# Kernel tuning notes

Measured on AMD Instinct MI355X. Metric: run time of the kernel, lower is better.

## Reference

```python
import math
import jax, jax.numpy as jnp
import numpy as np

HIDDEN = 1280
N_HEADS = 10
HEAD_DIM = HIDDEN // N_HEADS  # 128
ROPE_BASE = 10000.0
EPS = 1e-5


def _rope_freqs(head_dim, base):
    half = head_dim // 2
    return -jnp.exp(jnp.arange(0.0, half, dtype=jnp.float32) * (math.log(base) / half))


def apply_rotary_emb(x, offset=0, freqs=None):
    # x: (B, H, T, D), blocked (non-interleaved) RoPE layout
    B, H, T, D = x.shape
    if freqs is None:
        freqs = _rope_freqs(D, ROPE_BASE)
    positions = jnp.arange(offset, offset + T, dtype=jnp.float32)
    angles = jnp.outer(positions, freqs)          # (T, D/2)
    cos = jnp.cos(angles)
    sin = jnp.sin(angles)
    x1 = x[..., : D // 2]
    x2 = x[..., D // 2 :]
    rx1 = x1 * cos - x2 * sin
    rx2 = x2 * cos + x1 * sin
    return jnp.concatenate([rx1, rx2], axis=-1)


def rms_norm(x):
    return x * jax.lax.rsqrt(jnp.mean(jnp.square(x), axis=-1, keepdims=True) + EPS)


def setup_inputs() -> dict:
    key = jax.random.key(0)
    ks = jax.random.split(key, 5)
    B, L = 4, 2048
    s = 1.0 / math.sqrt(HIDDEN)
    return {
        "x": jax.random.normal(ks[0], (B, L, HIDDEN), dtype=jnp.float32),
        "wq": jax.random.normal(ks[1], (HIDDEN, HIDDEN), dtype=jnp.float32) * s,
        "wk": jax.random.normal(ks[2], (HIDDEN, HIDDEN), dtype=jnp.float32) * s,
        "wv": jax.random.normal(ks[3], (HIDDEN, HIDDEN), dtype=jnp.float32) * s,
        "wo": jax.random.normal(ks[4], (HIDDEN, HIDDEN), dtype=jnp.float32) * s,
    }


def reference(x, wq, wk, wv, wo):
    B, L, _ = x.shape
    scale = HEAD_DIM ** -0.5
    # QKV projections (Linear with weight W: y = x @ W.T)
    q = (x @ wq.T).reshape(B, L, N_HEADS, HEAD_DIM).transpose(0, 2, 1, 3)  # (B,H,L,D)
    k = (x @ wk.T).reshape(B, L, N_HEADS, HEAD_DIM).transpose(0, 2, 1, 3)
    v = (x @ wv.T).reshape(B, L, N_HEADS, HEAD_DIM).transpose(0, 2, 1, 3)
    freqs = _rope_freqs(HEAD_DIM, ROPE_BASE)
    q = rms_norm(apply_rotary_emb(q, 0, freqs))
    k = rms_norm(apply_rotary_emb(k, 0, freqs))
    # SDPA (no mask, matching mask=None path)
    scores = jnp.einsum("bhqd,bhkd->bhqk", q, k) * scale
    attn = jax.nn.softmax(scores, axis=-1)
    out = jnp.einsum("bhqk,bhkd->bhqd", attn, v)
    out = out.transpose(0, 2, 1, 3).reshape(B, L, HIDDEN)
    return out @ wo.T
```

## Files before the change

kernel.cpp:

```cpp
#include <hip/hip_runtime.h>
#include <math.h>

typedef unsigned short u16;
typedef unsigned long long u64;
typedef __attribute__((ext_vector_type(8))) short bf16x8;
typedef __attribute__((ext_vector_type(4))) float f32x4;
typedef __attribute__((ext_vector_type(4))) unsigned short u16x4;

#define MFMA16(a,b,c) __builtin_amdgcn_mfma_f32_16x16x32_bf16((a),(b),(c),0,0,0)

static constexpr int kHid = 1280;
static constexpr int kSeq = 2048;
static constexpr int kNH  = 10;
static constexpr int kHD  = 128;
static constexpr int kB   = 4;
static constexpr int kBL  = kB * kSeq;

__device__ __forceinline__ u16 f2bf(float f) {
  union { float f; unsigned u; } a; a.f = f;
  unsigned r = a.u + 0x7fffu + ((a.u >> 16) & 1u);
  return (u16)(r >> 16);
}
__device__ __forceinline__ float bf2f(u16 h) {
  union { unsigned u; float f; } a; a.u = ((unsigned)h) << 16;
  return a.f;
}

__device__ __forceinline__ void gll16(const void* g, void* l) {
  __builtin_amdgcn_global_load_lds((__attribute__((address_space(1))) void*)(g),
                                   (__attribute__((address_space(3))) void*)(l), 16, 0, 0);
}

__global__ __launch_bounds__(256) void cvt_bf16(const float* __restrict__ s,
                                                u16* __restrict__ d, int n4) {
  int i = blockIdx.x * 256 + threadIdx.x;
  if (i >= n4) return;
  float4 v = ((const float4*)s)[i];
  u16x4 o;
  o.x = f2bf(v.x); o.y = f2bf(v.y); o.z = f2bf(v.z); o.w = f2bf(v.w);
  ((u16x4*)d)[i] = o;
}

__global__ __launch_bounds__(256) void cvt_split(const float* __restrict__ s,
                                                 u16* __restrict__ dh,
                                                 u16* __restrict__ dl, int n4) {
  int i = blockIdx.x * 256 + threadIdx.x;
  if (i >= n4) return;
  float4 v = ((const float4*)s)[i];
  u16x4 oh, ol;
  oh.x = f2bf(v.x); ol.x = f2bf(v.x - bf2f(oh.x));
  oh.y = f2bf(v.y); ol.y = f2bf(v.y - bf2f(oh.y));
  oh.z = f2bf(v.z); ol.z = f2bf(v.z - bf2f(oh.z));
  oh.w = f2bf(v.w); ol.w = f2bf(v.w - bf2f(oh.w));
  ((u16x4*)dh)[i] = oh;
  ((u16x4*)dl)[i] = ol;
}

__device__ __forceinline__ double frac_of(int d, float* rout) {
  const float C = (float)(9.210340371976184 / 64.0);
  float a = (float)d * C;
  double e = exp((double)a);
  float r = (float)e;
  double fr;
  if (e >= (double)r) {
    float up = __int_as_float(__float_as_int(r) + 1);
    fr = (e - (double)r) / ((double)up - (double)r);
  } else {
    float dn = __int_as_float(__float_as_int(r) - 1);
    fr = (e - (double)r) / ((double)r - (double)dn);
  }
  *rout = r;
  return fr;
}

__global__ __launch_bounds__(256) void rope_tab(float* __restrict__ ct, float* __restrict__ st) {
  int i = blockIdx.x * 256 + threadIdx.x;
  if (i >= kSeq * 64) return;
  int t = i >> 6, d = i & 63;

  int dF = -1; double bm = 0.40; float rF = 1.0f;
  for (int dd = 38; dd <= 58; dd++) {
    float rr; double fr = frac_of(dd, &rr);
    if (fabs(fr) > bm) { bm = fabs(fr); dF = dd; rF = rr; }
  }
  const int binF = (dF >= 0) ? ilogbf(rF) : -9999;

  float r; double fr = frac_of(d, &r);
  double w = 0.0;
  if (d != dF && ilogbf(r) == binF) {
    double af = fabs(fr);
    w = (af >= 0.03 && af <= 0.32) ? 0.472 : 0.35;
  }
  int dir = (fr >= 0.0) ? 1 : -1;
  float rB = __int_as_float(__float_as_int(r) + dir);

  float A  = (float)t * (-r);
  float A2 = (float)t * (-rB);
  float c  = cosf(A),  s  = sinf(A);
  float c2 = cosf(A2), s2 = sinf(A2);
  float wf = (float)w;
  ct[i] = c + wf * (c2 - c);
  st[i] = s + wf * (s2 - s);
}

__global__ __launch_bounds__(256) void gemm_qkv(
    const u16* __restrict__ Ah, const u16* __restrict__ Al,
    const u16* __restrict__ Wh, const u16* __restrict__ Wl,
    const float* __restrict__ ct, const float* __restrict__ st,
    u16* __restrict__ qh, u16* __restrict__ ql,
    u16* __restrict__ kh, u16* __restrict__ kl,
    u16* __restrict__ vt)
{
  __shared__ u16 Ash[128 * 32];
  __shared__ u16 Bsh[128 * 32];
  __shared__ u16 Asl[128 * 32];
  __shared__ u16 Bsl[128 * 32];
  const int tid = threadIdx.x;
  const int w = tid >> 6, lane = tid & 63;
  const int c15 = lane & 15, q8 = lane >> 4;
  const int m0 = blockIdx.y * 128;
  const int bn = blockIdx.x;
  const int n0 = bn * 128;
  const bool split = (bn < 20);

  const f32x4 vzero = {0.f, 0.f, 0.f, 0.f};
  f32x4 acc[2][8];
#pragma unroll
  for (int i = 0; i < 2; i++)
#pragma unroll
    for (int j = 0; j < 8; j++) acc[i][j] = vzero;

  const int sr = w * 32 + (lane >> 2);
  const int sc = lane & 3;

  for (int k0 = 0; k0 < kHid; k0 += 32) {
#pragma unroll
    for (int i = 0; i < 2; i++) {
      int r = sr + i * 16;
      int gc = (sc ^ ((r >> 1) & 3)) << 3;
      size_t ga = (size_t)(m0 + r) * kHid + k0 + gc;
      size_t gb = (size_t)(n0 + r) * kHid + k0 + gc;
      gll16(Ah + ga, &Ash[(w * 32 + i * 16) * 32]);
      gll16(Wh + gb, &Bsh[(w * 32 + i * 16) * 32]);
      if (split) {
        gll16(Al + ga, &Asl[(w * 32 + i * 16) * 32]);
        gll16(Wl + gb, &Bsl[(w * 32 + i * 16) * 32]);
      }
    }
    __syncthreads();
    bf16x8 a0h, a1h, a0l, a1l;
    { int r = w * 32 + c15;      int o = r * 32 + ((q8 ^ ((r >> 1) & 3)) << 3);
      a0h = *(const bf16x8*)&Ash[o]; if (split) a0l = *(const bf16x8*)&Asl[o]; }
    { int r = w * 32 + 16 + c15; int o = r * 32 + ((q8 ^ ((r >> 1) & 3)) << 3);
      a1h = *(const bf16x8*)&Ash[o]; if (split) a1l = *(const bf16x8*)&Asl[o]; }
#pragma unroll
    for (int ni = 0; ni < 8; ni++) {
      int rb = ni * 16 + c15;
      int ob = rb * 32 + ((q8 ^ ((rb >> 1) & 3)) << 3);
      bf16x8 bbh = *(const bf16x8*)&Bsh[ob];
      acc[0][ni] = MFMA16(a0h, bbh, acc[0][ni]);
      acc[1][ni] = MFMA16(a1h, bbh, acc[1][ni]);
      if (split) {
        bf16x8 bbl = *(const bf16x8*)&Bsl[ob];
        acc[0][ni] = MFMA16(a0h, bbl, acc[0][ni]);
        acc[1][ni] = MFMA16(a1h, bbl, acc[1][ni]);
        acc[0][ni] = MFMA16(a0l, bbh, acc[0][ni]);
        acc[1][ni] = MFMA16(a1l, bbh, acc[1][ni]);
      }
    }
    __syncthreads();
  }

  const int typ = bn / 10, h = bn % 10;
#pragma unroll
  for (int mi = 0; mi < 2; mi++) {
#pragma unroll
    for (int rg = 0; rg < 4; rg++) {
      int n = m0 + w * 32 + mi * 16 + q8 * 4 + rg;
      int b = n >> 11, t = n & 2047;
      if (typ == 2) {
        size_t base = ((size_t)(b * kNH + h) * kHD) * kSeq + t;
#pragma unroll
        for (int ni = 0; ni < 8; ni++) {
          int d = ni * 16 + c15;
          vt[base + (size_t)d * kSeq] = f2bf(acc[mi][ni][rg]);
        }
      } else {
        float rv[8]; float ss = 0.f;
#pragma unroll
        for (int ni = 0; ni < 4; ni++) {
          int d = ni * 16 + c15;
          float cs = ct[t * 64 + d], sn = st[t * 64 + d];
          float x1 = acc[mi][ni][rg], x2 = acc[mi][ni + 4][rg];
          float r1 = x1 * cs - x2 * sn;
          float r2 = x2 * cs + x1 * sn;
          rv[ni] = r1; rv[ni + 4] = r2;
          ss += r1 * r1 + r2 * r2;
        }
#pragma unroll
        for (int off = 1; off < 16; off <<= 1) ss += __shfl_xor(ss, off, 64);
        float sc2 = rsqrtf(ss * (1.f / 128.f) + 1e-5f);
        u16* dsth = (typ == 0) ? qh : kh;
        u16* dstl = (typ == 0) ? ql : kl;
        size_t base = ((size_t)(b * kNH + h) * kSeq + t) * kHD;
#pragma unroll
        for (int ni = 0; ni < 8; ni++) {
          float val = rv[ni] * sc2;
          u16 hi = f2bf(val);
          dsth[base + ni * 16 + c15] = hi;
          dstl[base + ni * 16 + c15] = f2bf(val - bf2f(hi));
        }
      }
    }
  }
}

__global__ __launch_bounds__(256, 2) void attn_fwd(
    const u16* __restrict__ qhp, const u16* __restrict__ qlp,
    const u16* __restrict__ khp, const u16* __restrict__ klp,
    const u16* __restrict__ vt, u16* __restrict__ ao)
{
  __shared__ __align__(16) u16 smem[3 * 64 * 128];
  u16* const Ksh = smem;
  u16* const Ksl = smem + 64 * 128;
  u16* const Vs  = smem + 2 * 64 * 128;
  u16* const Ps  = smem;
  const int tid = threadIdx.x;
  const int w = tid >> 6, lane = tid & 63;
  const int c15 = lane & 15, q8 = lane >> 4;
  const int qt = blockIdx.x;
  const int bh = blockIdx.y;
  const int b = bh / kNH, h = bh % kNH;
  const size_t kvbase = (size_t)bh * kSeq * kHD;
  const int qr0 = qt * 128 + w * 32;

  bf16x8 qfh[4][2], qfl[4][2];
#pragma unroll
  for (int kd = 0; kd < 4; kd++)
#pragma unroll
    for (int mi = 0; mi < 2; mi++) {
      size_t off = kvbase + (size_t)(qr0 + mi * 16 + c15) * kHD + kd * 32 + q8 * 8;
      qfh[kd][mi] = *(const bf16x8*)&qhp[off];
      qfl[kd][mi] = *(const bf16x8*)&qlp[off];
    }

  const f32x4 vzero = {0.f, 0.f, 0.f, 0.f};
  f32x4 oacc[2][8];
#pragma unroll
  for (int i = 0; i < 2; i++)
#pragma unroll
    for (int j = 0; j < 8; j++) oacc[i][j] = vzero;
  float ms[2][4], ls[2][4];
#pragma unroll
  for (int i = 0; i < 2; i++)
#pragma unroll
    for (int j = 0; j < 4; j++) { ms[i][j] = -3.0e38f; ls[i][j] = 0.f; }

  const float SL2E = 0.08838834764831845f * 1.4426950408889634f;

  for (int kt = 0; kt < kSeq / 64; kt++) {
    const int kv0 = kt * 64;
#pragma unroll
    for (int i = 0; i < 4; i++) {
      int r = w * 16 + i * 4 + (lane >> 4);
      size_t g = kvbase + (size_t)(kv0 + r) * kHD + (((lane & 15) ^ (r & 7)) << 3);
      gll16(khp + g, &Ksh[(w * 16 + i * 4) * 128]);
      gll16(klp + g, &Ksl[(w * 16 + i * 4) * 128]);
    }
#pragma unroll
    for (int i = 0; i < 4; i++) {
      int d = w * 32 + i * 8 + (lane >> 3);
      gll16(vt + kvbase + (size_t)d * kSeq + kv0 + (((lane & 7) ^ (d & 7)) << 3),
            &Vs[(w * 32 + i * 8) * 64]);
    }
    __syncthreads();

    f32x4 sacc[2][4];
#pragma unroll
    for (int i = 0; i < 2; i++)
#pragma unroll
      for (int j = 0; j < 4; j++) sacc[i][j] = vzero;
    __builtin_amdgcn_s_setprio(1);
#pragma unroll
    for (int kd = 0; kd < 4; kd++) {
#pragma unroll
      for (int nk = 0; nk < 4; nk++) {
        int rb = nk * 16 + c15;
        int ob = rb * 128 + ((((kd << 2) + q8) ^ (rb & 7)) << 3);
        bf16x8 kbh = *(const bf16x8*)&Ksh[ob];
        bf16x8 kbl = *(const bf16x8*)&Ksl[ob];
        sacc[0][nk] = MFMA16(qfh[kd][0], kbh, sacc[0][nk]);
        sacc[0][nk] = MFMA16(qfh[kd][0], kbl, sacc[0][nk]);
        sacc[0][nk] = MFMA16(qfl[kd][0], kbh, sacc[0][nk]);
        sacc[1][nk] = MFMA16(qfh[kd][1], kbh, sacc[1][nk]);
        sacc[1][nk] = MFMA16(qfh[kd][1], kbl, sacc[1][nk]);
        sacc[1][nk] = MFMA16(qfl[kd][1], kbh, sacc[1][nk]);
      }
    }
    __builtin_amdgcn_s_setprio(0);
    __syncthreads();

#pragma unroll
    for (int mi = 0; mi < 2; mi++) {
#pragma unroll
      for (int rg = 0; rg < 4; rg++) {
        float v0 = sacc[mi][0][rg] * SL2E;
        float v1 = sacc[mi][1][rg] * SL2E;
        float v2 = sacc[mi][2][rg] * SL2E;
        float v3 = sacc[mi][3][rg] * SL2E;
        float mt = fmaxf(fmaxf(v0, v1), fmaxf(v2, v3));
#pragma unroll
        for (int off = 1; off < 16; off <<= 1) mt = fmaxf(mt, __shfl_xor(mt, off, 64));
        float mold = ms[mi][rg];
        float mnew = fmaxf(mold, mt);
        float alpha = exp2f(mold - mnew);
        float p0 = exp2f(v0 - mnew), p1 = exp2f(v1 - mnew);
        float p2 = exp2f(v2 - mnew), p3 = exp2f(v3 - mnew);
        float psum = (p0 + p1) + (p2 + p3);
#pragma unroll
        for (int off = 1; off < 16; off <<= 1) psum += __shfl_xor(psum, off, 64);
        ls[mi][rg] = ls[mi][rg] * alpha + psum;
        ms[mi][rg] = mnew;
#pragma unroll
        for (int nd = 0; nd < 8; nd++) oacc[mi][nd][rg] = oacc[mi][nd][rg] * alpha;
        int pr = w * 32 + mi * 16 + q8 * 4 + rg;
        Ps[pr * 72 +      c15] = f2bf(p0);
        Ps[pr * 72 + 16 + c15] = f2bf(p1);
        Ps[pr * 72 + 32 + c15] = f2bf(p2);
        Ps[pr * 72 + 48 + c15] = f2bf(p3);
      }
    }

    __builtin_amdgcn_s_setprio(1);
#pragma unroll
    for (int kk = 0; kk < 2; kk++) {
      bf16x8 pa0 = *(const bf16x8*)&Ps[(w * 32 + c15) * 72 + kk * 32 + q8 * 8];
      bf16x8 pa1 = *(const bf16x8*)&Ps[(w * 32 + 16 + c15) * 72 + kk * 32 + q8 * 8];
#pragma unroll
      for (int nd = 0; nd < 8; nd++) {
        int d = nd * 16 + c15;
        bf16x8 vb = *(const bf16x8*)&Vs[d * 64 + ((((kk << 2) + q8) ^ (d & 7)) << 3)];
        oacc[0][nd] = MFMA16(pa0, vb, oacc[0][nd]);
        oacc[1][nd] = MFMA16(pa1, vb, oacc[1][nd]);
      }
    }
    __builtin_amdgcn_s_setprio(0);
    __syncthreads();
  }

#pragma unroll
  for (int mi = 0; mi < 2; mi++) {
#pragma unroll
    for (int rg = 0; rg < 4; rg++) {
      int t = qr0 + mi * 16 + q8 * 4 + rg;
      float inv = 1.0f / ls[mi][rg];
      size_t base = ((size_t)(b * kSeq + t)) * kHid + h * kHD;
#pragma unroll
      for (int nd = 0; nd < 8; nd++)
        ao[base + nd * 16 + c15] = f2bf(oacc[mi][nd][rg] * inv);
    }
  }
}

__global__ __launch_bounds__(256) void gemm_out(
    const u16* __restrict__ A, const u16* __restrict__ Bw, float* __restrict__ out)
{
  __shared__ u16 As[128 * 32];
  __shared__ u16 Bs[128 * 32];
  const int tid = threadIdx.x;
  const int w = tid >> 6, lane = tid & 63;
  const int c15 = lane & 15, q8 = lane >> 4;
  const int m0 = blockIdx.y * 128;
  const int n0 = blockIdx.x * 128;

  const f32x4 vzero = {0.f, 0.f, 0.f, 0.f};
  f32x4 acc[2][8];
#pragma unroll
  for (int i = 0; i < 2; i++)
#pragma unroll
    for (int j = 0; j < 8; j++) acc[i][j] = vzero;

  const int sr = w * 32 + (lane >> 2);
  const int sc = lane & 3;

  for (int k0 = 0; k0 < kHid; k0 += 32) {
#pragma unroll
    for (int i = 0; i < 2; i++) {
      int r = sr + i * 16;
      int gc = (sc ^ ((r >> 1) & 3)) << 3;
      gll16(A  + (size_t)(m0 + r) * kHid + k0 + gc, &As[(w * 32 + i * 16) * 32]);
      gll16(Bw + (size_t)(n0 + r) * kHid + k0 + gc, &Bs[(w * 32 + i * 16) * 32]);
    }
    __syncthreads();
    bf16x8 a0, a1;
    { int r = w * 32 + c15;      a0 = *(const bf16x8*)&As[r * 32 + ((q8 ^ ((r >> 1) & 3)) << 3)]; }
    { int r = w * 32 + 16 + c15; a1 = *(const bf16x8*)&As[r * 32 + ((q8 ^ ((r >> 1) & 3)) << 3)]; }
#pragma unroll
    for (int ni = 0; ni < 8; ni++) {
      int rb = ni * 16 + c15;
      bf16x8 bb = *(const bf16x8*)&Bs[rb * 32 + ((q8 ^ ((rb >> 1) & 3)) << 3)];
      acc[0][ni] = MFMA16(a0, bb, acc[0][ni]);
      acc[1][ni] = MFMA16(a1, bb, acc[1][ni]);
    }
    __syncthreads();
  }

#pragma unroll
  for (int mi = 0; mi < 2; mi++) {
#pragma unroll
    for (int rg = 0; rg < 4; rg++) {
      int n = m0 + w * 32 + mi * 16 + q8 * 4 + rg;
      float* orow = out + (size_t)n * kHid + n0;
#pragma unroll
      for (int ni = 0; ni < 8; ni++) orow[ni * 16 + c15] = acc[mi][ni][rg];
    }
  }
}

extern "C" void kernel_launch(void* const* d_in, const int* in_sizes, int n_in,
                              void* d_out, int out_size, void* d_ws, size_t ws_size,
                              hipStream_t stream) {
  (void)in_sizes; (void)n_in; (void)out_size; (void)ws_size;
  const float* x  = (const float*)d_in[0];
  const float* wq = (const float*)d_in[1];
  const float* wk = (const float*)d_in[2];
  const float* wv = (const float*)d_in[3];
  const float* wo = (const float*)d_in[4];
  float* out = (float*)d_out;

  u16* xh    = (u16*)d_ws;
  u16* xl    = xh    + (size_t)kBL * kHid;
  u16* wqkvh = xl    + (size_t)kBL * kHid;
  u16* wqkl  = wqkvh + (size_t)3 * kHid * kHid;
  u16* woh   = wqkl  + (size_t)2 * kHid * kHid;
  u16* qhb   = woh   + (size_t)kHid * kHid;
  u16* qlb   = qhb   + (size_t)kB * kNH * kSeq * kHD;
  u16* khb   = qlb   + (size_t)kB * kNH * kSeq * kHD;
  u16* klb   = khb   + (size_t)kB * kNH * kSeq * kHD;
  u16* vtb   = klb   + (size_t)kB * kNH * kSeq * kHD;
  u16* aob   = vtb   + (size_t)kB * kNH * kSeq * kHD;
  float* ct  = (float*)(aob + (size_t)kBL * kHid);
  float* st  = ct + (size_t)kSeq * 64;

  const int n4x = kBL * kHid / 4;
  const int n4w = kHid * kHid / 4;
  cvt_split<<<(n4x + 255) / 256, 256, 0, stream>>>(x, xh, xl, n4x);
  cvt_split<<<(n4w + 255) / 256, 256, 0, stream>>>(wq, wqkvh, wqkl, n4w);
  cvt_split<<<(n4w + 255) / 256, 256, 0, stream>>>(wk, wqkvh + (size_t)kHid * kHid,
                                                  wqkl + (size_t)kHid * kHid, n4w);
  cvt_bf16<<<(n4w + 255) / 256, 256, 0, stream>>>(wv, wqkvh + (size_t)2 * kHid * kHid, n4w);
  cvt_bf16<<<(n4w + 255) / 256, 256, 0, stream>>>(wo, woh, n4w);
  rope_tab<<<(kSeq * 64 + 255) / 256, 256, 0, stream>>>(ct, st);

  gemm_qkv<<<dim3(30, 64), 256, 0, stream>>>(xh, xl, wqkvh, wqkl, ct, st,
                                             qhb, qlb, khb, klb, vtb);
  attn_fwd<<<dim3(16, 40), 256, 0, stream>>>(qhb, qlb, khb, klb, vtb, aob);
  gemm_out<<<dim3(10, 64), 256, 0, stream>>>(aob, woh, out);
}
```

Baseline: 825.8 us.

## Enlarge QKV GEMM tile to 128x256 with 512 threads and cross-wave RMS reduction

The QKV projection GEMM now uses 512-thread blocks that each compute a 128x256 output tile covering two heads, instead of 256-thread blocks with 128x128 tiles. Each wave computes a 64x64 sub-tile with a 4x4 accumulator grid, which raises arithmetic intensity per LDS load. The head-dimension split across waves means the RMS-norm sum of squares is now reduced through shared memory with an extra barrier. The launch grid uses 16 columns and the 16th column exits early. That idle column wastes slots, and the larger tile reduces the number of blocks, which may hurt occupancy.

```diff
diff --git a/kernel.cpp b/kernel.cpp
--- a/kernel.cpp
+++ b/kernel.cpp
@@ -103,7 +103,7 @@
   st[i] = s + wf * (s2 - s);
 }
 
-__global__ __launch_bounds__(256) void gemm_qkv(
+__global__ __launch_bounds__(512) void gemm_qkv(
     const u16* __restrict__ Ah, const u16* __restrict__ Al,
     const u16* __restrict__ Wh, const u16* __restrict__ Wl,
     const float* __restrict__ ct, const float* __restrict__ st,
@@ -112,103 +112,151 @@
     u16* __restrict__ vt)
 {
   __shared__ u16 Ash[128 * 32];
-  __shared__ u16 Bsh[128 * 32];
   __shared__ u16 Asl[128 * 32];
-  __shared__ u16 Bsl[128 * 32];
+  __shared__ u16 Bsh[256 * 32];
+  __shared__ u16 Bsl[256 * 32];
+  const int p = blockIdx.x;
+  if (p >= 15) return;
   const int tid = threadIdx.x;
   const int w = tid >> 6, lane = tid & 63;
   const int c15 = lane & 15, q8 = lane >> 4;
+  const int wr = w >> 2, wc = w & 3;
+  const int hsel = wc >> 1, hlo = wc & 1;
   const int m0 = blockIdx.y * 128;
-  const int bn = blockIdx.x;
-  const int n0 = bn * 128;
-  const bool split = (bn < 20);
+  const int typ = p / 5, pl = p % 5;
+  const int wrow0 = typ * kHid + pl * 256;
+  const bool split = (typ < 2);
 
   const f32x4 vzero = {0.f, 0.f, 0.f, 0.f};
-  f32x4 acc[2][8];
-#pragma unroll
-  for (int i = 0; i < 2; i++)
-#pragma unroll
-    for (int j = 0; j < 8; j++) acc[i][j] = vzero;
-
-  const int sr = w * 32 + (lane >> 2);
-  const int sc = lane & 3;
+  f32x4 acc[4][4];
+#pragma unroll
+  for (int i = 0; i < 4; i++)
+#pragma unroll
+    for (int j = 0; j < 4; j++) acc[i][j] = vzero;
+
+  const int srA = lane >> 2;
+  const int sc  = lane & 3;
 
   for (int k0 = 0; k0 < kHid; k0 += 32) {
-#pragma unroll
-    for (int i = 0; i < 2; i++) {
-      int r = sr + i * 16;
+    { int r = w * 16 + srA;
       int gc = (sc ^ ((r >> 1) & 3)) << 3;
       size_t ga = (size_t)(m0 + r) * kHid + k0 + gc;
-      size_t gb = (size_t)(n0 + r) * kHid + k0 + gc;
-      gll16(Ah + ga, &Ash[(w * 32 + i * 16) * 32]);
+      gll16(Ah + ga, &Ash[(w * 16) * 32]);
+      if (split) gll16(Al + ga, &Asl[(w * 16) * 32]);
+    }
+#pragma unroll
+    for (int i = 0; i < 2; i++) {
+      int r = w * 32 + i * 16 + srA;
+      int gc = (sc ^ ((r >> 1) & 3)) << 3;
+      size_t gb = (size_t)(wrow0 + r) * kHid + k0 + gc;
       gll16(Wh + gb, &Bsh[(w * 32 + i * 16) * 32]);
+      if (split) gll16(Wl + gb, &Bsl[(w * 32 + i * 16) * 32]);
+    }
+    __syncthreads();
+
+    bf16x8 ah[4], al[4];
+#pragma unroll
+    for (int m = 0; m < 4; m++) {
+      int r = wr * 64 + m * 16 + c15;
+      int o = r * 32 + ((q8 ^ ((r >> 1) & 3)) << 3);
+      ah[m] = *(const bf16x8*)&Ash[o];
+      if (split) al[m] = *(const bf16x8*)&Asl[o];
+    }
+#pragma unroll
+    for (int n = 0; n < 4; n++) {
+      int rb = hsel * 128 + (n >> 1) * 64 + hlo * 32 + (n & 1) * 16 + c15;
+      int ob = rb * 32 + ((q8 ^ ((rb >> 1) & 3)) << 3);
+      bf16x8 bh_ = *(const bf16x8*)&Bsh[ob];
       if (split) {
-        gll16(Al + ga, &Asl[(w * 32 + i * 16) * 32]);
-        gll16(Wl + gb, &Bsl[(w * 32 + i * 16) * 32]);
-      }
-    }
-    __syncthreads();
-    bf16x8 a0h, a1h, a0l, a1l;
-    { int r = w * 32 + c15;      int o = r * 32 + ((q8 ^ ((r >> 1) & 3)) << 3);
-      a0h = *(const bf16x8*)&Ash[o]; if (split) a0l = *(const bf16x8*)&Asl[o]; }
-    { int r = w * 32 + 16 + c15; int o = r * 32 + ((q8 ^ ((r >> 1) & 3)) << 3);
-      a1h = *(const bf16x8*)&Ash[o]; if (split) a1l = *(const bf16x8*)&Asl[o]; }
-#pragma unroll
-    for (int ni = 0; ni < 8; ni++) {
-      int rb = ni * 16 + c15;
-      int ob = rb * 32 + ((q8 ^ ((rb >> 1) & 3)) << 3);
-      bf16x8 bbh = *(const bf16x8*)&Bsh[ob];
-      acc[0][ni] = MFMA16(a0h, bbh, acc[0][ni]);
-      acc[1][ni] = MFMA16(a1h, bbh, acc[1][ni]);
-      if (split) {
-        bf16x8 bbl = *(const bf16x8*)&Bsl[ob];
-        acc[0][ni] = MFMA16(a0h, bbl, acc[0][ni]);
-        acc[1][ni] = MFMA16(a1h, bbl, acc[1][ni]);
-        acc[0][ni] = MFMA16(a0l, bbh, acc[0][ni]);
-        acc[1][ni] = MFMA16(a1l, bbh, acc[1][ni]);
-      }
-    }
-    __syncthreads();
-  }
-
-  const int typ = bn / 10, h = bn % 10;
-#pragma unroll
-  for (int mi = 0; mi < 2; mi++) {
-#pragma unroll
-    for (int rg = 0; rg < 4; rg++) {
-      int n = m0 + w * 32 + mi * 16 + q8 * 4 + rg;
-      int b = n >> 11, t = n & 2047;
-      if (typ == 2) {
-        size_t base = ((size_t)(b * kNH + h) * kHD) * kSeq + t;
-#pragma unroll
-        for (int ni = 0; ni < 8; ni++) {
-          int d = ni * 16 + c15;
-          vt[base + (size_t)d * kSeq] = f2bf(acc[mi][ni][rg]);
+        bf16x8 bl_ = *(const bf16x8*)&Bsl[ob];
+#pragma unroll
+        for (int m = 0; m < 4; m++) {
+          acc[m][n] = MFMA16(ah[m], bh_, acc[m][n]);
+          acc[m][n] = MFMA16(ah[m], bl_, acc[m][n]);
+          acc[m][n] = MFMA16(al[m], bh_, acc[m][n]);
         }
       } else {
-        float rv[8]; float ss = 0.f;
-#pragma unroll
-        for (int ni = 0; ni < 4; ni++) {
-          int d = ni * 16 + c15;
+#pragma unroll
+        for (int m = 0; m < 4; m++)
+          acc[m][n] = MFMA16(ah[m], bh_, acc[m][n]);
+      }
+    }
+    __syncthreads();
+  }
+
+  const int h = pl * 2 + hsel;
+  if (typ == 2) {
+#pragma unroll
+    for (int m = 0; m < 4; m++) {
+#pragma unroll
+      for (int rg = 0; rg < 4; rg++) {
+        int ntok = m0 + wr * 64 + m * 16 + q8 * 4 + rg;
+        int b = ntok >> 11, t = ntok & 2047;
+        size_t base = ((size_t)(b * kNH + h) * kHD) * kSeq + t;
+#pragma unroll
+        for (int n = 0; n < 4; n++) {
+          int d = (n >> 1) * 64 + hlo * 32 + (n & 1) * 16 + c15;
+          vt[base + (size_t)d * kSeq] = f2bf(acc[m][n][rg]);
+        }
+      }
+    }
+  } else {
+    float ssp[4][4];
+#pragma unroll
+    for (int m = 0; m < 4; m++) {
+#pragma unroll
+      for (int rg = 0; rg < 4; rg++) {
+        int ntok = m0 + wr * 64 + m * 16 + q8 * 4 + rg;
+        int t = ntok & 2047;
+        float ss = 0.f;
+#pragma unroll
+        for (int n = 0; n < 2; n++) {
+          int d = hlo * 32 + n * 16 + c15;
           float cs = ct[t * 64 + d], sn = st[t * 64 + d];
-          float x1 = acc[mi][ni][rg], x2 = acc[mi][ni + 4][rg];
+          float x1 = acc[m][n][rg], x2 = acc[m][n + 2][rg];
           float r1 = x1 * cs - x2 * sn;
           float r2 = x2 * cs + x1 * sn;
-          rv[ni] = r1; rv[ni + 4] = r2;
+          acc[m][n][rg] = r1; acc[m][n + 2][rg] = r2;
           ss += r1 * r1 + r2 * r2;
         }
 #pragma unroll
         for (int off = 1; off < 16; off <<= 1) ss += __shfl_xor(ss, off, 64);
-        float sc2 = rsqrtf(ss * (1.f / 128.f) + 1e-5f);
-        u16* dsth = (typ == 0) ? qh : kh;
-        u16* dstl = (typ == 0) ? ql : kl;
+        ssp[m][rg] = ss;
+      }
+    }
+    float* sbuf = (float*)Ash;
+    if (c15 == 0) {
+#pragma unroll
+      for (int m = 0; m < 4; m++)
+#pragma unroll
+        for (int rg = 0; rg < 4; rg++) {
+          int row = wr * 64 + m * 16 + q8 * 4 + rg;
+          sbuf[(hsel * 128 + row) * 2 + hlo] = ssp[m][rg];
+        }
+    }
+    __syncthreads();
+    u16* dsth = (typ == 0) ? qh : kh;
+    u16* dstl = (typ == 0) ? ql : kl;
+#pragma unroll
+    for (int m = 0; m < 4; m++) {
+#pragma unroll
+      for (int rg = 0; rg < 4; rg++) {
+        int row = wr * 64 + m * 16 + q8 * 4 + rg;
+        int ntok = m0 + row;
+        int b = ntok >> 11, t = ntok & 2047;
+        float sst = sbuf[(hsel * 128 + row) * 2] + sbuf[(hsel * 128 + row) * 2 + 1];
+        float sc2 = rsqrtf(sst * (1.f / 128.f) + 1e-5f);
         size_t base = ((size_t)(b * kNH + h) * kSeq + t) * kHD;
 #pragma unroll
-        for (int ni = 0; ni < 8; ni++) {
-          float val = rv[ni] * sc2;
-          u16 hi = f2bf(val);
-          dsth[base + ni * 16 + c15] = hi;
-          dstl[base + ni * 16 + c15] = f2bf(val - bf2f(hi));
+        for (int n = 0; n < 2; n++) {
+          int d = hlo * 32 + n * 16 + c15;
+          float v1 = acc[m][n][rg] * sc2;
+          float v2 = acc[m][n + 2][rg] * sc2;
+          u16 h1 = f2bf(v1), h2 = f2bf(v2);
+          dsth[base + d]      = h1;
+          dstl[base + d]      = f2bf(v1 - bf2f(h1));
+          dsth[base + d + 64] = h2;
+          dstl[base + d + 64] = f2bf(v2 - bf2f(h2));
         }
       }
     }
@@ -452,7 +500,7 @@
   cvt_bf16<<<(n4w + 255) / 256, 256, 0, stream>>>(wo, woh, n4w);
   rope_tab<<<(kSeq * 64 + 255) / 256, 256, 0, stream>>>(ct, st);
 
-  gemm_qkv<<<dim3(30, 64), 256, 0, stream>>>(xh, xl, wqkvh, wqkl, ct, st,
+  gemm_qkv<<<dim3(16, 64), 512, 0, stream>>>(xh, xl, wqkvh, wqkl, ct, st,
                                              qhb, qlb, khb, klb, vtb);
   attn_fwd<<<dim3(16, 40), 256, 0, stream>>>(qhb, qlb, khb, klb, vtb, aob);
   gemm_out<<<dim3(10, 64), 256, 0, stream>>>(aob, woh, out);
```

Measured after the change: 861.3 us. +4.3%, slower.
